# Performance work log

Measured on AMD Instinct MI355X. Metric: run time of the kernel, lower is better.

The kernel has to match this reference:

```python
import jax, jax.numpy as jnp
import numpy as np

TOP_K = 2  # routing_method: renormalize top-2 (topk then softmax over selected logits)


def setup_inputs() -> dict:
    key = jax.random.key(0)
    ks = jax.random.split(key, 5)
    T, H, I, E = 4096, 1024, 4096, 8
    return {
        "hidden_states": jax.random.normal(ks[0], (T, H), jnp.float32),
        "router_logits": jax.random.normal(ks[1], (T, E), jnp.float32),
        "W_gate": jax.random.normal(ks[2], (E, H, I), jnp.float32) * 0.02,  # w1
        "W_up": jax.random.normal(ks[3], (E, H, I), jnp.float32) * 0.02,   # w3
        "W_down": jax.random.normal(ks[4], (E, I, H), jnp.float32) * 0.02, # w2
    }


def reference(hidden_states, router_logits, W_gate, W_up, W_down):
    # Routing: top-k logits, renormalize with softmax over selected logits.
    top_vals, top_idx = jax.lax.top_k(router_logits, TOP_K)        # [T, K]
    routing_weights = jax.nn.softmax(top_vals, axis=-1)            # [T, K]

    E = W_gate.shape[0]
    out = jnp.zeros_like(hidden_states)                            # [T, H]
    for e in range(E):  # fixed small expert loop (structurally distinct weights)
        # combine weight for expert e per token (0 if not routed here)
        w_e = jnp.sum(jnp.where(top_idx == e, routing_weights, 0.0), axis=-1)  # [T]
        gate = hidden_states @ W_gate[e]                           # [T, I]
        up = hidden_states @ W_up[e]                               # [T, I]
        y = (jax.nn.silu(gate) * up) @ W_down[e]                   # [T, H]
        out = out + w_e[:, None] * y
    return out
```

## Files before the change

### kernel.cpp

```cpp
#include <hip/hip_runtime.h>

typedef float    f32x4 __attribute__((ext_vector_type(4)));
typedef _Float16 f16x8 __attribute__((ext_vector_type(8)));
typedef _Float16 f16x4 __attribute__((ext_vector_type(4)));

#define T_TOK 4096
#define HD    1024
#define ID    4096
#define NE    8
#define TOTP  (2*T_TOK)
#define BM    128
#define BN    128
#define MAXTILES 72

#define WS_CNT   0
#define WS_FILL  64
#define WS_OFF   128
#define WS_TOT   192
#define WS_TEXP  256
#define WS_TM0   (256 + 4*MAXTILES)
#define WS_TOPE  1024
#define WS_TOPW  (WS_TOPE + 4*TOTP)
#define WS_PAIR  (WS_TOPW + 4*TOTP)
#define WS_ACT   ((size_t)1 << 20)
constexpr size_t WS_YBUF = WS_ACT  + 2ull*TOTP*ID;
constexpr size_t WS_HS16 = WS_YBUF + 2ull*TOTP*HD;
constexpr size_t WS_WG16 = WS_HS16 + 2ull*T_TOK*HD;
constexpr size_t WS_WU16 = WS_WG16 + 2ull*NE*HD*ID;
constexpr size_t WS_WD16 = WS_WU16 + 2ull*NE*HD*ID;

__device__ __forceinline__ void gll16(const void* g, void* l) {
  __builtin_amdgcn_global_load_lds(
      (const __attribute__((address_space(1))) unsigned int*)g,
      (__attribute__((address_space(3))) unsigned int*)l, 16, 0, 0);
}

__device__ __forceinline__ int lofs(int row, int g) {
  return row * 32 + ((g ^ ((row >> 1) & 3)) << 3);
}
__device__ __forceinline__ int lofs64(int row, int g8) {
  return row * 64 + ((g8 ^ (row & 7)) << 3);
}

__global__ void k_router(const float* __restrict__ logits, char* __restrict__ ws) {
  int t = blockIdx.x * blockDim.x + threadIdx.x;
  if (t >= T_TOK) return;
  float v0 = -1e30f, v1 = -1e30f; int i0 = 0, i1 = 0;
  #pragma unroll
  for (int e = 0; e < NE; ++e) {
    float v = logits[t * NE + e];
    if (v > v0)      { v1 = v0; i1 = i0; v0 = v; i0 = e; }
    else if (v > v1) { v1 = v;  i1 = e; }
  }
  float w0 = 1.f / (1.f + __expf(v1 - v0));
  ((int*)(ws + WS_TOPE))[2*t]   = i0;
  ((int*)(ws + WS_TOPE))[2*t+1] = i1;
  ((float*)(ws + WS_TOPW))[2*t]   = w0;
  ((float*)(ws + WS_TOPW))[2*t+1] = 1.f - w0;
  atomicAdd(&((int*)(ws + WS_CNT))[i0], 1);
  atomicAdd(&((int*)(ws + WS_CNT))[i1], 1);
}

__global__ void k_prefix(char* __restrict__ ws) {
  if (threadIdx.x != 0 || blockIdx.x != 0) return;
  const int* cnt = (const int*)(ws + WS_CNT);
  int* off  = (int*)(ws + WS_OFF);
  int* texp = (int*)(ws + WS_TEXP);
  int* tm0  = (int*)(ws + WS_TM0);
  int run = 0, tiles = 0;
  for (int e = 0; e < NE; ++e) {
    off[e] = run;
    int ne = cnt[e];
    for (int i = 0; i < ne; i += BM) { texp[tiles] = e; tm0[tiles] = i; ++tiles; }
    run += ne;
  }
  off[NE] = run;
  *(int*)(ws + WS_TOT) = tiles;
}

__global__ void k_scatter(char* __restrict__ ws) {
  int t = blockIdx.x * blockDim.x + threadIdx.x;
  if (t >= T_TOK) return;
  const int* tope = (const int*)(ws + WS_TOPE);
  const int* off  = (const int*)(ws + WS_OFF);
  int* fill = (int*)(ws + WS_FILL);
  int* pair = (int*)(ws + WS_PAIR);
  #pragma unroll
  for (int s = 0; s < 2; ++s) {
    int id = 2*t + s;
    int e = tope[id];
    int pos = off[e] + atomicAdd(&fill[e], 1);
    pair[pos] = id;
  }
}

__global__ void k_hscvt(const float* __restrict__ src, _Float16* __restrict__ dst) {
  int i = blockIdx.x * blockDim.x + threadIdx.x;
  f32x4 v = ((const f32x4*)src)[i];
  f16x4 o;
  #pragma unroll
  for (int j = 0; j < 4; ++j) o[j] = (_Float16)v[j];
  ((f16x4*)dst)[i] = o;
}

__global__ __launch_bounds__(256) void k_wtrans(const float* __restrict__ src,
                                                _Float16* __restrict__ dst,
                                                int K, int N) {
  const int e = blockIdx.z;
  const int n0 = blockIdx.x * 64, k0 = blockIdx.y * 64;
  const float* s = src + (size_t)e * K * N;
  _Float16* d = dst + (size_t)e * (size_t)K * N;
  __shared__ _Float16 t[64][68];
  const int tx = threadIdx.x & 15, ty = threadIdx.x >> 4;
  #pragma unroll
  for (int it = 0; it < 4; ++it) {
    int k = k0 + it*16 + ty;
    f32x4 v = *(const f32x4*)&s[(size_t)k * N + n0 + tx*4];
    #pragma unroll
    for (int j = 0; j < 4; ++j) t[tx*4 + j][it*16 + ty] = (_Float16)v[j];
  }
  __syncthreads();
  #pragma unroll
  for (int it = 0; it < 4; ++it) {
    int n = it*16 + ty;
    *(f16x4*)&d[(size_t)(n0 + n) * K + k0 + tx*4] = *(const f16x4*)&t[n][tx*4];
  }
}

__global__ __launch_bounds__(512) void k_gemm1(
    const _Float16* __restrict__ hs16, const _Float16* __restrict__ WgT,
    const _Float16* __restrict__ WuT, char* __restrict__ ws) {
  const int s = blockIdx.y;
  if (s >= *(const int*)(ws + WS_TOT)) return;
  const int e    = ((const int*)(ws + WS_TEXP))[s];
  const int m0   = ((const int*)(ws + WS_TM0))[s];
  const int offE = ((const int*)(ws + WS_OFF))[e];
  const int nE   = ((const int*)(ws + WS_CNT))[e];
  _Float16* __restrict__ act = (_Float16*)(ws + WS_ACT);
  const int n0 = blockIdx.x * BN;
  const int tid = threadIdx.x, lane = tid & 63, wid = tid >> 6;

  __shared__ __align__(16) _Float16 sm[2 * 3 * BM * 32];

  const int rL = lane >> 2;
  const int q  = (((lane & 3) ^ ((lane >> 3) & 3)) << 3);
  int tok;
  { int mm = m0 + 16*wid + rL;
    tok = (mm < nE) ? (((const int*)(ws + WS_PAIR))[offE + mm] >> 1) : 0; }
  const _Float16* aS = hs16 + (size_t)tok * HD + q;
  const int colB = n0 + 16*wid + rL;
  const _Float16* gS = WgT + ((size_t)e * ID + colB) * HD + q;
  const _Float16* uS = WuT + ((size_t)e * ID + colB) * HD + q;

  auto stage = [&](int buf, int kt) {
    _Float16* b = sm + buf * (3*BM*32) + wid * 512;
    const int ko = kt * 32;
    gll16(aS + ko, b);
    gll16(gS + ko, b + BM*32);
    gll16(uS + ko, b + 2*BM*32);
  };

  const int wr = wid >> 2, wc = wid & 3;
  const int l15 = lane & 15, l4 = lane >> 4;
  f32x4 accg[4][2] = {}, accu[4][2] = {};

  auto compute = [&](int buf) {
    const _Float16* b0 = sm + buf * (3*BM*32);
    f16x8 afr[4], gfr[2], ufr[2];
    #pragma unroll
    for (int i = 0; i < 4; ++i)
      afr[i] = *(const f16x8*)&b0[lofs(64*wr + 16*i + l15, l4)];
    #pragma unroll
    for (int j = 0; j < 2; ++j) {
      gfr[j] = *(const f16x8*)&b0[BM*32   + lofs(32*wc + 16*j + l15, l4)];
      ufr[j] = *(const f16x8*)&b0[2*BM*32 + lofs(32*wc + 16*j + l15, l4)];
    }
    #pragma unroll
    for (int i = 0; i < 4; ++i)
      #pragma unroll
      for (int j = 0; j < 2; ++j) {
        accg[i][j] = __builtin_amdgcn_mfma_f32_16x16x32_f16(afr[i], gfr[j], accg[i][j], 0, 0, 0);
        accu[i][j] = __builtin_amdgcn_mfma_f32_16x16x32_f16(afr[i], ufr[j], accu[i][j], 0, 0, 0);
      }
  };

  stage(0, 0);
  asm volatile("s_waitcnt vmcnt(0)" ::: "memory");
  __syncthreads();
  const int KT = HD / 32;
  for (int kt = 0; kt < KT; ++kt) {
    const int cur = kt & 1;
    if (kt + 1 < KT) stage(cur ^ 1, kt + 1);
    compute(cur);
    asm volatile("s_waitcnt vmcnt(0)" ::: "memory");
    __syncthreads();
  }

  #pragma unroll
  for (int i = 0; i < 4; ++i)
    #pragma unroll
    for (int r = 0; r < 4; ++r) {
      const int mm = m0 + 64*wr + 16*i + 4*l4 + r;
      if (mm < nE) {
        const size_t prow = (size_t)(offE + mm) * ID;
        #pragma unroll
        for (int j = 0; j < 2; ++j) {
          float g = accg[i][j][r], u = accu[i][j][r];
          float sv = g / (1.f + __expf(-g)) * u;
          act[prow + n0 + 32*wc + 16*j + l15] = (_Float16)sv;
        }
      }
    }
}

__global__ __launch_bounds__(512) void k_gemm2(const _Float16* __restrict__ WdT,
                                               char* __restrict__ ws) {
  const int s = blockIdx.y;
  if (s >= *(const int*)(ws + WS_TOT)) return;
  const int e    = ((const int*)(ws + WS_TEXP))[s];
  const int m0   = ((const int*)(ws + WS_TM0))[s];
  const int offE = ((const int*)(ws + WS_OFF))[e];
  const int nE   = ((const int*)(ws + WS_CNT))[e];
  const int* __restrict__ pair = (const int*)(ws + WS_PAIR);
  const _Float16* __restrict__ act = (const _Float16*)(ws + WS_ACT);
  _Float16* __restrict__ ybuf = (_Float16*)(ws + WS_YBUF);
  const int n0 = blockIdx.x * BN;
  const int tid = threadIdx.x, lane = tid & 63, wid = tid >> 6;

  __shared__ __align__(16) _Float16 sm[2 * 2 * BM * 64];

  const int rL8 = lane >> 3;
  const int q8  = (((lane & 7) ^ rL8) << 3);
  const int mmA0 = m0 + 16*wid + rL8, mmA1 = mmA0 + 8;
  const _Float16* aS0 = act + (size_t)(offE + (mmA0 < nE ? mmA0 : 0)) * ID + q8;
  const _Float16* aS1 = act + (size_t)(offE + (mmA1 < nE ? mmA1 : 0)) * ID + q8;
  const int cB = n0 + 16*wid + rL8;
  const _Float16* bS0 = WdT + ((size_t)e * HD + cB) * ID + q8;
  const _Float16* bS1 = bS0 + 8ull * ID;

  auto stage = [&](int buf, int kt) {
    _Float16* b = sm + buf * (2*BM*64) + wid * 1024;
    const int ko = kt * 64;
    gll16(aS0 + ko, b);
    gll16(aS1 + ko, b + 512);
    gll16(bS0 + ko, b + BM*64);
    gll16(bS1 + ko, b + BM*64 + 512);
  };

  const int wr = wid >> 2, wc = wid & 3;
  const int l15 = lane & 15, l4 = lane >> 4;
  f32x4 acc[4][2] = {};

  auto compute = [&](int buf) {
    const _Float16* b0 = sm + buf * (2*BM*64);
    #pragma unroll
    for (int ks = 0; ks < 2; ++ks) {
      f16x8 afr[4], bfr[2];
      #pragma unroll
      for (int i = 0; i < 4; ++i)
        afr[i] = *(const f16x8*)&b0[lofs64(64*wr + 16*i + l15, ks*4 + l4)];
      #pragma unroll
      for (int j = 0; j < 2; ++j)
        bfr[j] = *(const f16x8*)&b0[BM*64 + lofs64(32*wc + 16*j + l15, ks*4 + l4)];
      #pragma unroll
      for (int i = 0; i < 4; ++i)
        #pragma unroll
        for (int j = 0; j < 2; ++j)
          acc[i][j] = __builtin_amdgcn_mfma_f32_16x16x32_f16(afr[i], bfr[j], acc[i][j], 0, 0, 0);
    }
  };

  stage(0, 0);
  asm volatile("s_waitcnt vmcnt(0)" ::: "memory");
  __syncthreads();
  const int KT = ID / 64;
  for (int kt = 0; kt < KT; ++kt) {
    const int cur = kt & 1;
    if (kt + 1 < KT) stage(cur ^ 1, kt + 1);
    compute(cur);
    asm volatile("s_waitcnt vmcnt(0)" ::: "memory");
    __syncthreads();
  }

  #pragma unroll
  for (int i = 0; i < 4; ++i)
    #pragma unroll
    for (int r = 0; r < 4; ++r) {
      const int mm = m0 + 64*wr + 16*i + 4*l4 + r;
      if (mm < nE) {
        const int id = pair[offE + mm];
        #pragma unroll
        for (int j = 0; j < 2; ++j)
          ybuf[(size_t)id * HD + n0 + 32*wc + 16*j + l15] = (_Float16)acc[i][j][r];
      }
    }
}

__global__ void k_combine(const char* __restrict__ ws, float* __restrict__ out) {
  const int idx = blockIdx.x * blockDim.x + threadIdx.x;
  const int t = idx >> 7, c = idx & 127;
  const float* topw = (const float*)(ws + WS_TOPW);
  const _Float16* yb = (const _Float16*)(ws + WS_YBUF);
  f16x8 y0 = ((const f16x8*)(yb + (size_t)(2*t)     * HD))[c];
  f16x8 y1 = ((const f16x8*)(yb + (size_t)(2*t + 1) * HD))[c];
  const float w0 = topw[2*t], w1 = topw[2*t+1];
  f32x4 o0, o1;
  #pragma unroll
  for (int j = 0; j < 4; ++j) {
    o0[j] = w0 * (float)y0[j]     + w1 * (float)y1[j];
    o1[j] = w0 * (float)y0[4 + j] + w1 * (float)y1[4 + j];
  }
  ((f32x4*)out)[2*idx]     = o0;
  ((f32x4*)out)[2*idx + 1] = o1;
}

extern "C" void kernel_launch(void* const* d_in, const int* in_sizes, int n_in,
                              void* d_out, int out_size, void* d_ws, size_t ws_size,
                              hipStream_t stream) {
  const float* hs     = (const float*)d_in[0];
  const float* logits = (const float*)d_in[1];
  const float* Wg     = (const float*)d_in[2];
  const float* Wu     = (const float*)d_in[3];
  const float* Wd     = (const float*)d_in[4];
  char* ws = (char*)d_ws;

  _Float16* hs16 = (_Float16*)(ws + WS_HS16);
  _Float16* wg16 = (_Float16*)(ws + WS_WG16);
  _Float16* wu16 = (_Float16*)(ws + WS_WU16);
  _Float16* wd16 = (_Float16*)(ws + WS_WD16);

  hipMemsetAsync(ws, 0, 256, stream);
  k_router <<<dim3(T_TOK/256), dim3(256), 0, stream>>>(logits, ws);
  k_prefix <<<dim3(1),         dim3(64),  0, stream>>>(ws);
  k_scatter<<<dim3(T_TOK/256), dim3(256), 0, stream>>>(ws);
  k_hscvt  <<<dim3(T_TOK*HD/4/256), dim3(256), 0, stream>>>(hs, hs16);
  k_wtrans <<<dim3(ID/64, HD/64, NE), dim3(256), 0, stream>>>(Wg, wg16, HD, ID);
  k_wtrans <<<dim3(ID/64, HD/64, NE), dim3(256), 0, stream>>>(Wu, wu16, HD, ID);
  k_wtrans <<<dim3(HD/64, ID/64, NE), dim3(256), 0, stream>>>(Wd, wd16, ID, HD);
  k_gemm1  <<<dim3(ID/BN, MAXTILES), dim3(512), 0, stream>>>(hs16, wg16, wu16, ws);
  k_gemm2  <<<dim3(HD/BN, MAXTILES), dim3(512), 0, stream>>>(wd16, ws);
  k_combine<<<dim3(T_TOK*HD/8/256), dim3(256), 0, stream>>>(ws, (float*)d_out);
}
```

Baseline: 496.4 us.

## Triple-buffer LDS pipelines in both MoE GEMMs with partial vmcnt waits

Both expert GEMM kernels move from double-buffered LDS staging with a full vmcnt(0) wait each iteration to a three-stage ring. Each iteration issues loads two tiles ahead and waits only for the oldest group. The GEMM2 K-tile shrinks from 64 to 32 to match the GEMM1 layout and fit the third buffer, and MFMA blocks are wrapped in s_setprio to favour compute waves. The intent is to hide global-load latency behind MFMA work, at the cost of more LDS per block, which may lower occupancy, and of twice as many GEMM2 iterations and barriers.

Result: no change. 490.3 us (-1.2%).

```diff
diff --git a/kernel.cpp b/kernel.cpp
--- a/kernel.cpp
+++ b/kernel.cpp
@@ -35,11 +35,13 @@
       (__attribute__((address_space(3))) unsigned int*)l, 16, 0, 0);
 }
 
+#define WAITV(N) do { \
+    asm volatile("s_waitcnt vmcnt(" #N ")" ::: "memory"); \
+    __builtin_amdgcn_sched_barrier(0); \
+  } while (0)
+
 __device__ __forceinline__ int lofs(int row, int g) {
   return row * 32 + ((g ^ ((row >> 1) & 3)) << 3);
-}
-__device__ __forceinline__ int lofs64(int row, int g8) {
-  return row * 64 + ((g8 ^ (row & 7)) << 3);
 }
 
 __global__ void k_router(const float* __restrict__ logits, char* __restrict__ ws) {
@@ -140,7 +142,7 @@
   const int n0 = blockIdx.x * BN;
   const int tid = threadIdx.x, lane = tid & 63, wid = tid >> 6;
 
-  __shared__ __align__(16) _Float16 sm[2 * 3 * BM * 32];
+  __shared__ __align__(16) _Float16 sm[3 * 3 * BM * 32];
 
   const int rL = lane >> 2;
   const int q  = (((lane & 3) ^ ((lane >> 3) & 3)) << 3);
@@ -175,6 +177,7 @@
       gfr[j] = *(const f16x8*)&b0[BM*32   + lofs(32*wc + 16*j + l15, l4)];
       ufr[j] = *(const f16x8*)&b0[2*BM*32 + lofs(32*wc + 16*j + l15, l4)];
     }
+    __builtin_amdgcn_s_setprio(1);
     #pragma unroll
     for (int i = 0; i < 4; ++i)
       #pragma unroll
@@ -182,19 +185,25 @@
         accg[i][j] = __builtin_amdgcn_mfma_f32_16x16x32_f16(afr[i], gfr[j], accg[i][j], 0, 0, 0);
         accu[i][j] = __builtin_amdgcn_mfma_f32_16x16x32_f16(afr[i], ufr[j], accu[i][j], 0, 0, 0);
       }
+    __builtin_amdgcn_s_setprio(0);
   };
 
-  stage(0, 0);
-  asm volatile("s_waitcnt vmcnt(0)" ::: "memory");
-  __syncthreads();
   const int KT = HD / 32;
-  for (int kt = 0; kt < KT; ++kt) {
-    const int cur = kt & 1;
-    if (kt + 1 < KT) stage(cur ^ 1, kt + 1);
-    compute(cur);
-    asm volatile("s_waitcnt vmcnt(0)" ::: "memory");
-    __syncthreads();
-  }
+  stage(0, 0); stage(1, 1);
+  for (int t = 0; t < KT - 2; ++t) {
+    stage((t + 2) % 3, t + 2);
+    WAITV(6);
+    __builtin_amdgcn_s_barrier();
+    compute(t % 3);
+    __builtin_amdgcn_s_barrier();
+  }
+  WAITV(3);
+  __builtin_amdgcn_s_barrier();
+  compute((KT - 2) % 3);
+  __builtin_amdgcn_s_barrier();
+  WAITV(0);
+  __builtin_amdgcn_s_barrier();
+  compute((KT - 1) % 3);
 
   #pragma unroll
   for (int i = 0; i < 4; ++i)
@@ -227,24 +236,20 @@
   const int n0 = blockIdx.x * BN;
   const int tid = threadIdx.x, lane = tid & 63, wid = tid >> 6;
 
-  __shared__ __align__(16) _Float16 sm[2 * 2 * BM * 64];
-
-  const int rL8 = lane >> 3;
-  const int q8  = (((lane & 7) ^ rL8) << 3);
-  const int mmA0 = m0 + 16*wid + rL8, mmA1 = mmA0 + 8;
-  const _Float16* aS0 = act + (size_t)(offE + (mmA0 < nE ? mmA0 : 0)) * ID + q8;
-  const _Float16* aS1 = act + (size_t)(offE + (mmA1 < nE ? mmA1 : 0)) * ID + q8;
-  const int cB = n0 + 16*wid + rL8;
-  const _Float16* bS0 = WdT + ((size_t)e * HD + cB) * ID + q8;
-  const _Float16* bS1 = bS0 + 8ull * ID;
+  __shared__ __align__(16) _Float16 sm[3 * 2 * BM * 32];
+
+  const int rL = lane >> 2;
+  const int q  = (((lane & 3) ^ ((lane >> 3) & 3)) << 3);
+  int pA; { int mm = m0 + 16*wid + rL; pA = (mm < nE) ? (offE + mm) : 0; }
+  const _Float16* aS = act + (size_t)pA * ID + q;
+  const int cB = n0 + 16*wid + rL;
+  const _Float16* bS = WdT + ((size_t)e * HD + cB) * ID + q;
 
   auto stage = [&](int buf, int kt) {
-    _Float16* b = sm + buf * (2*BM*64) + wid * 1024;
-    const int ko = kt * 64;
-    gll16(aS0 + ko, b);
-    gll16(aS1 + ko, b + 512);
-    gll16(bS0 + ko, b + BM*64);
-    gll16(bS1 + ko, b + BM*64 + 512);
+    _Float16* b = sm + buf * (2*BM*32) + wid * 512;
+    const int ko = kt * 32;
+    gll16(aS + ko, b);
+    gll16(bS + ko, b + BM*32);
   };
 
   const int wr = wid >> 2, wc = wid & 3;
@@ -252,35 +257,39 @@
   f32x4 acc[4][2] = {};
 
   auto compute = [&](int buf) {
-    const _Float16* b0 = sm + buf * (2*BM*64);
-    #pragma unroll
-    for (int ks = 0; ks < 2; ++ks) {
-      f16x8 afr[4], bfr[2];
-      #pragma unroll
-      for (int i = 0; i < 4; ++i)
-        afr[i] = *(const f16x8*)&b0[lofs64(64*wr + 16*i + l15, ks*4 + l4)];
+    const _Float16* b0 = sm + buf * (2*BM*32);
+    f16x8 afr[4], bfr[2];
+    #pragma unroll
+    for (int i = 0; i < 4; ++i)
+      afr[i] = *(const f16x8*)&b0[lofs(64*wr + 16*i + l15, l4)];
+    #pragma unroll
+    for (int j = 0; j < 2; ++j)
+      bfr[j] = *(const f16x8*)&b0[BM*32 + lofs(32*wc + 16*j + l15, l4)];
+    __builtin_amdgcn_s_setprio(1);
+    #pragma unroll
+    for (int i = 0; i < 4; ++i)
       #pragma unroll
       for (int j = 0; j < 2; ++j)
-        bfr[j] = *(const f16x8*)&b0[BM*64 + lofs64(32*wc + 16*j + l15, ks*4 + l4)];
-      #pragma unroll
-      for (int i = 0; i < 4; ++i)
-        #pragma unroll
-        for (int j = 0; j < 2; ++j)
-          acc[i][j] = __builtin_amdgcn_mfma_f32_16x16x32_f16(afr[i], bfr[j], acc[i][j], 0, 0, 0);
-    }
+        acc[i][j] = __builtin_amdgcn_mfma_f32_16x16x32_f16(afr[i], bfr[j], acc[i][j], 0, 0, 0);
+    __builtin_amdgcn_s_setprio(0);
   };
 
-  stage(0, 0);
-  asm volatile("s_waitcnt vmcnt(0)" ::: "memory");
-  __syncthreads();
-  const int KT = ID / 64;
-  for (int kt = 0; kt < KT; ++kt) {
-    const int cur = kt & 1;
-    if (kt + 1 < KT) stage(cur ^ 1, kt + 1);
-    compute(cur);
-    asm volatile("s_waitcnt vmcnt(0)" ::: "memory");
-    __syncthreads();
-  }
+  const int KT = ID / 32;
+  stage(0, 0); stage(1, 1);
+  for (int t = 0; t < KT - 2; ++t) {
+    stage((t + 2) % 3, t + 2);
+    WAITV(4);
+    __builtin_amdgcn_s_barrier();
+    compute(t % 3);
+    __builtin_amdgcn_s_barrier();
+  }
+  WAITV(2);
+  __builtin_amdgcn_s_barrier();
+  compute((KT - 2) % 3);
+  __builtin_amdgcn_s_barrier();
+  WAITV(0);
+  __builtin_amdgcn_s_barrier();
+  compute((KT - 1) % 3);
 
   #pragma unroll
   for (int i = 0; i < 4; ++i)
```
